# Performance work log

Hardware: AMD Instinct MI355X
Metric: run time of the kernel (lower is better)

## Reference

```python
import jax, jax.numpy as jnp
import numpy as np

C_IN, C_OUT, K, H, W = 16, 16, 3, 1024, 1024
PAD = 1  # 'same' padding for 3x3 stride-1


def setup_inputs() -> dict:
    key = jax.random.key(0)
    kx, kw, kb = jax.random.split(key, 3)
    x = jax.random.normal(kx, (1, C_IN, H, W), dtype=jnp.float32)
    weight = jax.random.normal(kw, (C_OUT, C_IN, K, K), dtype=jnp.float32) * 0.05
    bias = jax.random.normal(kb, (C_OUT,), dtype=jnp.float32) * 0.05
    return {"x": x, "weight": weight, "bias": bias}


def reference(x, weight, bias):
    # Original module: im2col (unfold) + matmul + reshape + bias add.
    # Mathematically identical to a dense 2D convolution (cross-correlation),
    # expressed here as the fused implicit-GEMM conv primitive.
    out = jax.lax.conv_general_dilated(
        x, weight,
        window_strides=(1, 1),
        padding=((PAD, PAD), (PAD, PAD)),
        dimension_numbers=("NCHW", "OIHW", "NCHW"),
    )  # [1, C_OUT, H, W]
    # out_unf.view(*output_shape) drops the batch dim (batch must be 1)
    return out[0] + bias[:, None, None]
```

## Files before the change

kernel.cpp:

```cpp
#include <hip/hip_runtime.h>


#define HH 1024
#define WW 1024
#define CIN 16
#define COUT 16
#define TW 32
#define TH 16
#define NT 2
#define LROWS (TH + 2)
#define LCOLS (TW + 2)
#define PIX 16
#define NPIX (LROWS * LCOLS)
#define SMHALF (NPIX * PIX)

typedef short v8s __attribute__((ext_vector_type(8)));
typedef float v4f __attribute__((ext_vector_type(4)));
typedef unsigned int u32;

__device__ __forceinline__ unsigned short f32_bf16(float f) {
    union { float f; u32 u; } v;
    v.f = f;
    u32 u = v.u;
    u += 0x7fffu + ((u >> 16) & 1u);
    return (unsigned short)(u >> 16);
}

__device__ __forceinline__ u32 cvt_pk_bf16(float lo, float hi) {
    u32 r;
    asm("v_cvt_pk_bf16_f32 %0, %1, %2" : "=v"(r) : "v"(lo), "v"(hi));
    return r;
}

__device__ __forceinline__ int swz(int c) { return c ^ ((c >> 3) & 7); }

__global__ __launch_bounds__(256, 3)
void conv3x3_fused(const float* __restrict__ x,
                   const float* __restrict__ wgt,
                   const float* __restrict__ bias,
                   float* __restrict__ out) {
    __shared__ __align__(16) unsigned short sm[2 * SMHALF];
    __shared__ __align__(16) unsigned short wsm[20 * 16 * 8];

    const int tid = threadIdx.x;
    const int lane = tid & 63;
    const int wave = tid >> 6;
    const int h0blk = blockIdx.y * (TH * NT);
    const int w0 = blockIdx.x * TW;

    if (tid < 32) ((uint4*)(wsm + 18 * 16 * 8))[tid] = make_uint4(0u, 0u, 0u, 0u);
    #pragma unroll
    for (int s = 0; s < 9; ++s) {
        const int e = s * 256 + tid;
        const int m = e / 144;
        const int rem = e - m * 144;
        const int c = rem / 9;
        const int r9 = rem - c * 9;
        const int t = r9 * 2 + (c >> 3);
        wsm[(t * 16 + m) * 8 + (c & 7)] = f32_bf16(wgt[e]);
    }

    auto load_tile = [&](int t, float4* f4, float* fh) {
        const int h0 = h0blk + t * TH;
        if (tid < 144) {
            const int r = tid >> 3;
            const int j = tid & 7;
            const int gh = h0 - 1 + r;
            if ((unsigned)gh < (unsigned)HH) {
                const float4* src = (const float4*)(x + (size_t)gh * WW + w0) + j;
                #pragma unroll
                for (int c = 0; c < CIN; ++c)
                    f4[c] = src[(size_t)c * (HH * WW / 4)];
            } else {
                #pragma unroll
                for (int c = 0; c < CIN; ++c)
                    f4[c] = make_float4(0.f, 0.f, 0.f, 0.f);
            }
        } else if (tid < 180) {
            const int h = tid - 144;
            const int r = h >> 1;
            const int side = h & 1;
            const int gh = h0 - 1 + r;
            const int gw = side ? (w0 + TW) : (w0 - 1);
            if ((unsigned)gh < (unsigned)HH && (unsigned)gw < (unsigned)WW) {
                const float* src = x + (size_t)gh * WW + gw;
                #pragma unroll
                for (int c = 0; c < CIN; ++c) fh[c] = src[(size_t)c * (HH * WW)];
            } else {
                #pragma unroll
                for (int c = 0; c < CIN; ++c) fh[c] = 0.f;
            }
        }
    };
    auto write_tile = [&](int t, const float4* f4, const float* fh) {
        unsigned short* smb = sm + (t & 1) * SMHALF;
        if (tid < 144) {
            const int r = tid >> 3;
            const int j = tid & 7;
            const int pbase = r * LCOLS + 1 + 4 * j;
            #pragma unroll
            for (int k = 0; k < 4; ++k) {
                u32 pk[8];
                #pragma unroll
                for (int i = 0; i < 8; ++i) {
                    const float lo = ((const float*)&f4[2 * i])[k];
                    const float hi = ((const float*)&f4[2 * i + 1])[k];
                    pk[i] = cvt_pk_bf16(lo, hi);
                }
                #pragma unroll
                for (int half = 0; half < 2; ++half) {
                    const int cc = 2 * pbase + 2 * k + half;
                    *(uint4*)(smb + swz(cc) * 8) = *(uint4*)&pk[half * 4];
                }
            }
        } else if (tid < 180) {
            const int h = tid - 144;
            const int r = h >> 1;
            const int side = h & 1;
            const int p = r * LCOLS + (side ? (LCOLS - 1) : 0);
            u32 pk[8];
            #pragma unroll
            for (int i = 0; i < 8; ++i)
                pk[i] = cvt_pk_bf16(fh[2 * i], fh[2 * i + 1]);
            #pragma unroll
            for (int half = 0; half < 2; ++half) {
                const int cc = 2 * p + half;
                *(uint4*)(smb + swz(cc) * 8) = *(uint4*)&pk[half * 4];
            }
        }
    };

    const int m = lane & 15;
    const int q = lane >> 4;
    const int wc = wave & 1;
    const int wq = wave >> 1;
    const int colbase = wc * 16 + m;

    int Kofs[5];
    #pragma unroll
    for (int g5 = 0; g5 < 5; ++g5) {
        int t = 4 * g5 + q;
        int tt = t > 17 ? 17 : t;
        int khkw = tt >> 1;
        int kh = khkw / 3;
        int kw = khkw - 3 * kh;
        int half = tt & 1;
        Kofs[g5] = (kh * LCOLS + colbase + kw) * 2 + half;
    }
    float bl[4];
    #pragma unroll
    for (int i = 0; i < 4; ++i) bl[i] = bias[q * 4 + i];

    float4 fA[CIN]; float hA[CIN];
    float4 fB[CIN]; float hB[CIN];
    load_tile(0, fA, hA);
    write_tile(0, fA, hA);
    load_tile(1, fB, hB);
    __syncthreads();

    v8s a[5];
    #pragma unroll
    for (int g5 = 0; g5 < 5; ++g5) {
        const int t = 4 * g5 + q;
        a[g5] = *(const v8s*)(wsm + (t * 16 + m) * 8);
    }

    auto compute_tile = [&](int t) {
        const unsigned short* smb = sm + (t & 1) * SMHALF;
        const int h0 = h0blk + t * TH;
        #pragma unroll 4
        for (int rr = 0; rr < 8; ++rr) {
            const int r = wq * 8 + rr;
            v4f acc = {0.f, 0.f, 0.f, 0.f};
            #pragma unroll
            for (int g5 = 0; g5 < 5; ++g5) {
                const int c = r * (LCOLS * 2) + Kofs[g5];
                v8s b = *(const v8s*)(smb + swz(c) * 8);
                acc = __builtin_amdgcn_mfma_f32_16x16x32_bf16(a[g5], b, acc, 0, 0, 0);
            }
            float* op = out + (size_t)(h0 + r) * WW + (w0 + colbase);
            #pragma unroll
            for (int i = 0; i < 4; ++i)
                op[(size_t)(q * 4 + i) * (HH * WW)] = acc[i] + bl[i];
        }
    };

    compute_tile(0);
    write_tile(1, fB, hB);
    __syncthreads();
    compute_tile(1);
}

extern "C" void kernel_launch(void* const* d_in, const int* in_sizes, int n_in,
                              void* d_out, int out_size, void* d_ws, size_t ws_size,
                              hipStream_t stream) {
    const float* x = (const float*)d_in[0];
    const float* w = (const float*)d_in[1];
    const float* b = (const float*)d_in[2];
    float* out = (float*)d_out;
    dim3 grid(WW / TW, HH / (TH * NT));
    conv3x3_fused<<<grid, dim3(256), 0, stream>>>(x, w, b, out);
}
```

Before: 137.2 us.

## Retile to 64x8 strips with four-tile register-prefetched pipeline per block

Widens each tile to 64 columns by 8 rows and has every block process four consecutive tiles. The next tile's global loads are issued before the current shared-memory write and compute, so loads overlap with MFMA work across two alternating LDS buffers. Each wave now owns a 16-column strip over all rows, the halo loads are folded into the same register buffer, and the full __syncthreads is replaced by an LDS-only waitcnt plus s_barrier. In exchange, the occupancy hint drops from 3 to 2 blocks per CU, the grid halves, and vertical halo re-reads rise because tiles are only 8 rows tall.

```diff
diff --git a/kernel.cpp b/kernel.cpp
--- a/kernel.cpp
+++ b/kernel.cpp
@@ -5,9 +5,9 @@
 #define WW 1024
 #define CIN 16
 #define COUT 16
-#define TW 32
-#define TH 16
-#define NT 2
+#define TW 64
+#define TH 8
+#define NT 4
 #define LROWS (TH + 2)
 #define LCOLS (TW + 2)
 #define PIX 16
@@ -34,7 +34,15 @@
 
 __device__ __forceinline__ int swz(int c) { return c ^ ((c >> 3) & 7); }
 
-__global__ __launch_bounds__(256, 3)
+__device__ __forceinline__ void wave_barrier() {
+    __builtin_amdgcn_sched_barrier(0);
+    asm volatile("s_waitcnt lgkmcnt(0)" ::: "memory");
+    __builtin_amdgcn_sched_barrier(0);
+    __builtin_amdgcn_s_barrier();
+    __builtin_amdgcn_sched_barrier(0);
+}
+
+__global__ __launch_bounds__(256, 2)
 void conv3x3_fused(const float* __restrict__ x,
                    const float* __restrict__ wgt,
                    const float* __restrict__ bias,
@@ -60,11 +68,11 @@
         wsm[(t * 16 + m) * 8 + (c & 7)] = f32_bf16(wgt[e]);
     }
 
-    auto load_tile = [&](int t, float4* f4, float* fh) {
+    auto load_tile = [&](int t, float4* f4) {
         const int h0 = h0blk + t * TH;
-        if (tid < 144) {
-            const int r = tid >> 3;
-            const int j = tid & 7;
+        if (tid < 160) {
+            const int r = tid >> 4;
+            const int j = tid & 15;
             const int gh = h0 - 1 + r;
             if ((unsigned)gh < (unsigned)HH) {
                 const float4* src = (const float4*)(x + (size_t)gh * WW + w0) + j;
@@ -77,7 +85,8 @@
                     f4[c] = make_float4(0.f, 0.f, 0.f, 0.f);
             }
         } else if (tid < 180) {
-            const int h = tid - 144;
+            float* f = (float*)f4;
+            const int h = tid - 160;
             const int r = h >> 1;
             const int side = h & 1;
             const int gh = h0 - 1 + r;
@@ -85,18 +94,18 @@
             if ((unsigned)gh < (unsigned)HH && (unsigned)gw < (unsigned)WW) {
                 const float* src = x + (size_t)gh * WW + gw;
                 #pragma unroll
-                for (int c = 0; c < CIN; ++c) fh[c] = src[(size_t)c * (HH * WW)];
+                for (int c = 0; c < CIN; ++c) f[c] = src[(size_t)c * (HH * WW)];
             } else {
                 #pragma unroll
-                for (int c = 0; c < CIN; ++c) fh[c] = 0.f;
+                for (int c = 0; c < CIN; ++c) f[c] = 0.f;
             }
         }
     };
-    auto write_tile = [&](int t, const float4* f4, const float* fh) {
+    auto write_tile = [&](int t, const float4* f4) {
         unsigned short* smb = sm + (t & 1) * SMHALF;
-        if (tid < 144) {
-            const int r = tid >> 3;
-            const int j = tid & 7;
+        if (tid < 160) {
+            const int r = tid >> 4;
+            const int j = tid & 15;
             const int pbase = r * LCOLS + 1 + 4 * j;
             #pragma unroll
             for (int k = 0; k < 4; ++k) {
@@ -114,14 +123,15 @@
                 }
             }
         } else if (tid < 180) {
-            const int h = tid - 144;
+            const float* f = (const float*)f4;
+            const int h = tid - 160;
             const int r = h >> 1;
             const int side = h & 1;
             const int p = r * LCOLS + (side ? (LCOLS - 1) : 0);
             u32 pk[8];
             #pragma unroll
             for (int i = 0; i < 8; ++i)
-                pk[i] = cvt_pk_bf16(fh[2 * i], fh[2 * i + 1]);
+                pk[i] = cvt_pk_bf16(f[2 * i], f[2 * i + 1]);
             #pragma unroll
             for (int half = 0; half < 2; ++half) {
                 const int cc = 2 * p + half;
@@ -132,9 +142,7 @@
 
     const int m = lane & 15;
     const int q = lane >> 4;
-    const int wc = wave & 1;
-    const int wq = wave >> 1;
-    const int colbase = wc * 16 + m;
+    const int colbase = wave * 16 + m;
 
     int Kofs[5];
     #pragma unroll
@@ -151,12 +159,14 @@
     #pragma unroll
     for (int i = 0; i < 4; ++i) bl[i] = bias[q * 4 + i];
 
-    float4 fA[CIN]; float hA[CIN];
-    float4 fB[CIN]; float hB[CIN];
-    load_tile(0, fA, hA);
-    write_tile(0, fA, hA);
-    load_tile(1, fB, hB);
-    __syncthreads();
+    float4 pA[CIN];
+    float4 pB[CIN];
+    load_tile(0, pA);
+    write_tile(0, pA);
+    load_tile(1, pB);
+    __builtin_amdgcn_sched_barrier(0);
+
+    wave_barrier();
 
     v8s a[5];
     #pragma unroll
@@ -168,9 +178,8 @@
     auto compute_tile = [&](int t) {
         const unsigned short* smb = sm + (t & 1) * SMHALF;
         const int h0 = h0blk + t * TH;
-        #pragma unroll 4
-        for (int rr = 0; rr < 8; ++rr) {
-            const int r = wq * 8 + rr;
+        #pragma unroll
+        for (int r = 0; r < TH; ++r) {
             v4f acc = {0.f, 0.f, 0.f, 0.f};
             #pragma unroll
             for (int g5 = 0; g5 < 5; ++g5) {
@@ -183,12 +192,26 @@
             for (int i = 0; i < 4; ++i)
                 op[(size_t)(q * 4 + i) * (HH * WW)] = acc[i] + bl[i];
         }
+        __builtin_amdgcn_sched_barrier(0);
     };
 
     compute_tile(0);
-    write_tile(1, fB, hB);
-    __syncthreads();
+    load_tile(2, pA);
+    __builtin_amdgcn_sched_barrier(0);
+    write_tile(1, pB);
+    wave_barrier();
+
     compute_tile(1);
+    load_tile(3, pB);
+    __builtin_amdgcn_sched_barrier(0);
+    write_tile(2, pA);
+    wave_barrier();
+
+    compute_tile(2);
+    write_tile(3, pB);
+    wave_barrier();
+
+    compute_tile(3);
 }
 
 extern "C" void kernel_launch(void* const* d_in, const int* in_sizes, int n_in,
```

New measurement: 127.1 us. -7.4%, faster.
